# Performance work log

Hardware: AMD Instinct MI355X
Metric: run time of the kernel (lower is better)

Reference implementation:

```python
import jax, jax.numpy as jnp
import numpy as np

B, S, H, NH = 2, 1024, 1024, 16
SE, E = 512, 1024
NEXP, TOPK, FF = 8, 2, 2048
HD = H // NH
EPS = 1e-6
THETA = 10000.0
NEG = -1e9


def _rms(x, w):
    return x * jax.lax.rsqrt(jnp.mean(x * x, axis=-1, keepdims=True) + EPS) * w


def _rope(q, k, pos):
    # q,k: [B,S,NH,HD]; pos: [B,S] int
    inv = 1.0 / (THETA ** (jnp.arange(0, HD, 2, dtype=jnp.float32) / HD))
    f = pos[..., None].astype(jnp.float32) * inv            # [B,S,HD/2]
    emb = jnp.concatenate([f, f], axis=-1)                  # [B,S,HD]
    cos = jnp.cos(emb)[:, :, None, :]
    sin = jnp.sin(emb)[:, :, None, :]
    def rot(x):
        x1, x2 = jnp.split(x, 2, axis=-1)
        return jnp.concatenate([-x2, x1], axis=-1)
    return q * cos + rot(q) * sin, k * cos + rot(k) * sin


def _forward(hidden_states, encoder_hidden_states,
             in_ln_w, wq, wk, wv, wo,
             c_norm_w, cq_w, cq_b, ck_w, ck_b, cv_w, cv_b, co_w, co_b,
             post_ln_w, gate_w, w1, w2, w3,
             position_ids, encoder_attention_mask):
    x = hidden_states

    # ---- self-attention (RMSNorm pre-norm, RoPE, causal) ----
    res = x
    h = _rms(x, in_ln_w)
    q = (h @ wq.T).reshape(B, S, NH, HD)
    k = (h @ wk.T).reshape(B, S, NH, HD)
    v = (h @ wv.T).reshape(B, S, NH, HD)
    q, k = _rope(q, k, position_ids)
    scores = jnp.einsum('bqhd,bkhd->bhqk', q, k) / np.sqrt(HD)
    causal = jnp.tril(jnp.ones((S, S), dtype=bool))
    scores = jnp.where(causal, scores, NEG)
    attn = jax.nn.softmax(scores, axis=-1)
    o = jnp.einsum('bhqk,bkhd->bqhd', attn, v).reshape(B, S, H) @ wo.T
    x = res + o

    # ---- cross-attention block (RMSNorm, MHA with kdim=vdim=E, bias) ----
    res = x
    h = _rms(x, c_norm_w)
    cq = (h @ cq_w.T + cq_b).reshape(B, S, NH, HD)
    ck = (encoder_hidden_states @ ck_w.T + ck_b).reshape(B, SE, NH, HD)
    cv = (encoder_hidden_states @ cv_w.T + cv_b).reshape(B, SE, NH, HD)
    sc = jnp.einsum('bqhd,bkhd->bhqk', cq, ck) / np.sqrt(HD)
    pad = (encoder_attention_mask == 0)                     # key_padding_mask
    sc = jnp.where(pad[:, None, None, :], NEG, sc)
    ca = jax.nn.softmax(sc, axis=-1)
    o = jnp.einsum('bhqk,bkhd->bqhd', ca, cv).reshape(B, S, H) @ co_w.T + co_b
    x = res + o

    # ---- block-sparse MoE FFN (top-2 routing, SwiGLU experts) ----
    res = x
    h = _rms(x, post_ln_w).reshape(-1, H)                   # [T,H], T=B*S
    logits = h @ gate_w.T                                    # [T,NEXP]
    probs = jax.nn.softmax(logits, axis=-1)
    topv, topi = jax.lax.top_k(probs, TOPK)                  # [T,TOPK]
    topv = topv / jnp.sum(topv, axis=-1, keepdims=True)
    out = jnp.zeros_like(h)
    for e in range(NEXP):  # fixed small expert loop
        we = jnp.sum(jnp.where(topi == e, topv, 0.0), axis=-1)   # [T]
        ff = (jax.nn.silu(h @ w1[e].T) * (h @ w3[e].T)) @ w2[e].T
        out = out + we[:, None] * ff
    x = res + out.reshape(B, S, H)
    return x


def setup_inputs() -> dict:
    key = jax.random.key(0)
    ks = jax.random.split(key, 24)
    sc = 0.02
    d = {
        'hidden_states': jax.random.normal(ks[0], (B, S, H), jnp.float32),
        'position_ids': jnp.broadcast_to(jnp.arange(S, dtype=jnp.int64), (B, S)),
        'encoder_hidden_states': jax.random.normal(ks[1], (B, SE, E), jnp.float32),
        'encoder_attention_mask': jnp.ones((B, SE), jnp.int64),
        'in_ln_w': jnp.ones((H,), jnp.float32),
        'wq': jax.random.normal(ks[2], (H, H), jnp.float32) * sc,
        'wk': jax.random.normal(ks[3], (H, H), jnp.float32) * sc,
        'wv': jax.random.normal(ks[4], (H, H), jnp.float32) * sc,
        'wo': jax.random.normal(ks[5], (H, H), jnp.float32) * sc,
        'c_norm_w': jnp.ones((H,), jnp.float32),
        'cq_w': jax.random.normal(ks[6], (H, H), jnp.float32) * sc,
        'cq_b': jnp.zeros((H,), jnp.float32),
        'ck_w': jax.random.normal(ks[7], (H, E), jnp.float32) * sc,
        'ck_b': jnp.zeros((H,), jnp.float32),
        'cv_w': jax.random.normal(ks[8], (H, E), jnp.float32) * sc,
        'cv_b': jnp.zeros((H,), jnp.float32),
        'co_w': jax.random.normal(ks[9], (H, H), jnp.float32) * sc,
        'co_b': jnp.zeros((H,), jnp.float32),
        'post_ln_w': jnp.ones((H,), jnp.float32),
        'gate_w': jax.random.normal(ks[10], (NEXP, H), jnp.float32) * sc,
        'w1': jax.random.normal(ks[11], (NEXP, FF, H), jnp.float32) * sc,
        'w2': jax.random.normal(ks[12], (NEXP, H, FF), jnp.float32) * sc,
        'w3': jax.random.normal(ks[13], (NEXP, FF, H), jnp.float32) * sc,
    }
    return d


def reference(hidden_states, position_ids, encoder_hidden_states, encoder_attention_mask,
              in_ln_w, wq, wk, wv, wo,
              c_norm_w, cq_w, cq_b, ck_w, ck_b, cv_w, cv_b, co_w, co_b,
              post_ln_w, gate_w, w1, w2, w3):
    return _forward(hidden_states, encoder_hidden_states,
                    in_ln_w, wq, wk, wv, wo,
                    c_norm_w, cq_w, cq_b, ck_w, ck_b, cv_w, cv_b, co_w, co_b,
                    post_ln_w, gate_w, w1, w2, w3,
                    position_ids, encoder_attention_mask)
```

## Files before the change

kernel.cpp:

```cpp
#include <hip/hip_runtime.h>

#define B_    2
#define S_    1024
#define H_    1024
#define NH_   16
#define HD_   64
#define SE_   512
#define E_    1024
#define NEXP_ 8
#define FF_   2048
#define T_    (B_*S_)
#define TE_   (B_*SE_)
#define PERM_MAX 6400
#define MAXRT 24

typedef short v8s __attribute__((ext_vector_type(8)));
typedef short v4s __attribute__((ext_vector_type(4)));
typedef float v4f __attribute__((ext_vector_type(4)));
typedef _Float16 v8h __attribute__((ext_vector_type(8)));
typedef _Float16 v4h __attribute__((ext_vector_type(4)));

__device__ __forceinline__ unsigned short f2b(float f) {
  unsigned int u = __float_as_uint(f);
  u = (u + 0x7FFFu + ((u >> 16) & 1u)) >> 16;
  return (unsigned short)u;
}

__device__ __forceinline__ void g2l16(const void* g, void* l) {
  __builtin_amdgcn_global_load_lds(
      (const __attribute__((address_space(1))) unsigned int*)g,
      (__attribute__((address_space(3))) unsigned int*)l, 16, 0, 0);
}

__global__ void detect_kern(const int* __restrict__ pos, const int* __restrict__ msk,
                            int* __restrict__ flags) {
  if (threadIdx.x == 0) {
    flags[0] = (pos[1] == 1) ? 0 : 1;
    flags[1] = (msk[1] == 1) ? 0 : 1;
  }
}

struct SplitArgs {
  const float* src[9];
  _Float16* dh[9];
  _Float16* dl[9];
};
__global__ __launch_bounds__(256)
void split_all(SplitArgs sa) {
  int b = blockIdx.x;
  int seg, i;
  if (b < 4096) { seg = b >> 9; i = (b & 511) * 256 + threadIdx.x; }
  else          { seg = 8;      i = (b - 4096) * 256 + threadIdx.x; }
  const float* x = sa.src[seg];
  v4f a = *(const v4f*)&x[i * 8];
  v4f c = *(const v4f*)&x[i * 8 + 4];
  v8h hv, lv;
  #pragma unroll
  for (int j = 0; j < 8; ++j) {
    float v = j < 4 ? a[j] : c[j - 4];
    _Float16 hh = (_Float16)v;
    hv[j] = hh; lv[j] = (_Float16)(v - (float)hh);
  }
  *(v8h*)&sa.dh[seg][i * 8] = hv;
  *(v8h*)&sa.dl[seg][i * 8] = lv;
}

__global__ __launch_bounds__(256)
void cvt_all(const float* __restrict__ s0, const float* __restrict__ s1,
             const float* __restrict__ s2,
             unsigned short* __restrict__ d0, unsigned short* __restrict__ d1,
             unsigned short* __restrict__ d2) {
  int b = blockIdx.x;
  int seg = b >> 14;
  int i = (b & 16383) * 256 + threadIdx.x;
  const float* x = seg == 0 ? s0 : (seg == 1 ? s1 : s2);
  unsigned short* y = seg == 0 ? d0 : (seg == 1 ? d1 : d2);
  v4f v = *(const v4f*)&x[i * 4];
  v4s o;
  #pragma unroll
  for (int j = 0; j < 4; ++j) o[j] = (short)f2b(v[j]);
  *(v4s*)&y[i * 4] = o;
}

__global__ __launch_bounds__(256)
void rmsnorm_hl_kern(const float* __restrict__ x, const float* __restrict__ w,
                     _Float16* __restrict__ yh, _Float16* __restrict__ yl) {
  int row = blockIdx.x, tid = threadIdx.x;
  const float* xr = x + (long)row * 1024;
  v4f v = *(const v4f*)&xr[tid * 4];
  float ss = v[0]*v[0] + v[1]*v[1] + v[2]*v[2] + v[3]*v[3];
  #pragma unroll
  for (int off = 32; off; off >>= 1) ss += __shfl_xor(ss, off);
  __shared__ float sw[4];
  if ((tid & 63) == 0) sw[tid >> 6] = ss;
  __syncthreads();
  float tot = sw[0] + sw[1] + sw[2] + sw[3];
  float rs = rsqrtf(tot * (1.0f / 1024.0f) + 1e-6f);
  const float* wr = w + tid * 4;
  v4h oh, ol;
  #pragma unroll
  for (int j = 0; j < 4; ++j) {
    float f = v[j] * rs * wr[j];
    _Float16 hh = (_Float16)f;
    oh[j] = hh; ol[j] = (_Float16)(f - (float)hh);
  }
  *(v4h*)&yh[(long)row * 1024 + tid * 4] = oh;
  *(v4h*)&yl[(long)row * 1024 + tid * 4] = ol;
}

__global__ __launch_bounds__(256)
void rmsnorm_kern(const float* __restrict__ x, const float* __restrict__ w,
                  unsigned short* __restrict__ y) {
  int row = blockIdx.x, tid = threadIdx.x;
  const float* xr = x + (long)row * 1024;
  v4f v = *(const v4f*)&xr[tid * 4];
  float ss = v[0]*v[0] + v[1]*v[1] + v[2]*v[2] + v[3]*v[3];
  #pragma unroll
  for (int off = 32; off; off >>= 1) ss += __shfl_xor(ss, off);
  __shared__ float sw[4];
  if ((tid & 63) == 0) sw[tid >> 6] = ss;
  __syncthreads();
  float tot = sw[0] + sw[1] + sw[2] + sw[3];
  float rs = rsqrtf(tot * (1.0f / 1024.0f) + 1e-6f);
  const float* wr = w + tid * 4;
  v4s o;
  #pragma unroll
  for (int j = 0; j < 4; ++j) o[j] = (short)f2b(v[j] * rs * wr[j]);
  *(v4s*)&y[(long)row * 1024 + tid * 4] = o;
}

__global__ __launch_bounds__(256)
void rope_split_kern(float* __restrict__ q, const float* __restrict__ k,
                     _Float16* __restrict__ kh, _Float16* __restrict__ kl,
                     const int* __restrict__ pos, const int* __restrict__ flags) {
  int g = blockIdx.x * 256 + threadIdx.x;
  int d = g & 31;
  int h = (g >> 5) & 15;
  int s = (g >> 9) & (S_ - 1);
  int b = g >> 19;
  long base = (((long)(b * S_ + s)) * NH_ + h) * HD_;
  int pidx = b * S_ + s;
  int pv = pos[flags[0] ? (pidx << 1) : pidx];
  float p = (float)pv;
  float inv = powf(10000.0f, -(float)d * (1.0f / 32.0f));
  float f = p * inv;
  float sn = sinf(f), cs = cosf(f);
  float q1 = q[base + d], q2 = q[base + d + 32];
  q[base + d]      = q1 * cs - q2 * sn;
  q[base + d + 32] = q2 * cs + q1 * sn;
  float k1 = k[base + d], k2 = k[base + d + 32];
  float kr1 = k1 * cs - k2 * sn;
  float kr2 = k2 * cs + k1 * sn;
  _Float16 hh = (_Float16)kr1;
  kh[base + d] = hh; kl[base + d] = (_Float16)(kr1 - (float)hh);
  hh = (_Float16)kr2;
  kh[base + d + 32] = hh; kl[base + d + 32] = (_Float16)(kr2 - (float)hh);
}

__global__ __launch_bounds__(256)
void vtrans_kern(const float* __restrict__ vf, _Float16* __restrict__ vth,
                 _Float16* __restrict__ vtl, int Sk) {
  int kb = blockIdx.x, bh = blockIdx.y;
  int b = bh >> 4, h = bh & 15;
  int t = threadIdx.x;
  __shared__ float tile[64][65];
  int key = t >> 2, dsub = (t & 3) * 16;
  const float* src = vf + (((long)(b * Sk + kb * 64 + key)) * NH_ + h) * HD_ + dsub;
  #pragma unroll
  for (int j = 0; j < 16; j += 4) *(v4f*)&tile[key][dsub + j] = *(const v4f*)&src[j];
  __syncthreads();
  int d = t >> 2, ksub = (t & 3) * 16;
  v8h hv0, lv0, hv1, lv1;
  #pragma unroll
  for (int j = 0; j < 16; ++j) {
    float v = tile[ksub + j][d];
    _Float16 hh = (_Float16)v;
    if (j < 8) { hv0[j] = hh; lv0[j] = (_Float16)(v - (float)hh); }
    else       { hv1[j - 8] = hh; lv1[j - 8] = (_Float16)(v - (float)hh); }
  }
  long ob = (((long)(b * NH_ + h)) * HD_ + d) * Sk + kb * 64 + ksub;
  *(v8h*)&vth[ob] = hv0; *(v8h*)&vth[ob + 8] = hv1;
  *(v8h*)&vtl[ob] = lv0; *(v8h*)&vtl[ob + 8] = lv1;
}

struct ZArg {
  const _Float16 *Ah, *Al, *Bh, *Bl;
  const float *bias, *resid;
  float *Cf;
  _Float16 *Ch, *Cl;
  int M;
};

__global__ __launch_bounds__(256)
void gemm_hl(ZArg z0, ZArg z1, ZArg z2, int K) {
  ZArg za = blockIdx.z == 0 ? z0 : (blockIdx.z == 1 ? z1 : z2);
  int flat = blockIdx.x;
  int wg = (flat & 7) * 32 + (flat >> 3);
  int row0 = (wg >> 4) * 128;
  int col0 = (wg & 15) * 64;
  if (row0 >= za.M) return;
  int tid = threadIdx.x, lane = tid & 63, w = tid >> 6;
  int lr = lane & 15, lg = lane >> 4;
  int wr = w >> 1, wc = w & 1;
  int rsw = (lr >> 1) & 3;

  __shared__ _Float16 Ah_s[2][128 * 32], Al_s[2][128 * 32];
  __shared__ _Float16 Bh_s[2][64 * 32], Bl_s[2][64 * 32];

  int av0 = w * 64 + lane, av1 = (w + 4) * 64 + lane;
  int ar0 = av0 >> 2, as0 = (av0 & 3) ^ ((ar0 >> 1) & 3);
  int ar1 = av1 >> 2, as1 = (av1 & 3) ^ ((ar1 >> 1) & 3);
  int bv = w * 64 + lane;
  int br = bv >> 2, bs = (bv & 3) ^ ((br >> 1) & 3);
  const _Float16* ga0h = za.Ah + (long)(row0 + ar0) * K + as0 * 8;
  const _Float16* ga0l = za.Al + (long)(row0 + ar0) * K + as0 * 8;
  const _Float16* ga1h = za.Ah + (long)(row0 + ar1) * K + as1 * 8;
  const _Float16* ga1l = za.Al + (long)(row0 + ar1) * K + as1 * 8;
  const _Float16* gbh  = za.Bh + (long)(col0 + br) * K + bs * 8;
  const _Float16* gbl  = za.Bl + (long)(col0 + br) * K + bs * 8;

  auto stage = [&](int buf, int k0) {
    g2l16(ga0h + k0, (char*)Ah_s[buf] + w * 1024);
    g2l16(ga1h + k0, (char*)Ah_s[buf] + (w + 4) * 1024);
    g2l16(ga0l + k0, (char*)Al_s[buf] + w * 1024);
    g2l16(ga1l + k0, (char*)Al_s[buf] + (w + 4) * 1024);
    g2l16(gbh + k0, (char*)Bh_s[buf] + w * 1024);
    g2l16(gbl + k0, (char*)Bl_s[buf] + w * 1024);
  };

  v4f acc[4][2] = {};
  stage(0, 0);
  int cur = 0;

  for (int k0 = 0; k0 < K; k0 += 32) {
    __syncthreads();
    if (k0 + 32 < K) stage(cur ^ 1, k0 + 32);

    v8h ah[4], al[4], bh[2], bl[2];
    #pragma unroll
    for (int m = 0; m < 4; ++m) {
      int off = (wr * 64 + m * 16 + lr) * 64 + ((lg ^ rsw) << 4);
      ah[m] = *(const v8h*)((char*)Ah_s[cur] + off);
      al[m] = *(const v8h*)((char*)Al_s[cur] + off);
    }
    #pragma unroll
    for (int n = 0; n < 2; ++n) {
      int off = (wc * 32 + n * 16 + lr) * 64 + ((lg ^ rsw) << 4);
      bh[n] = *(const v8h*)((char*)Bh_s[cur] + off);
      bl[n] = *(const v8h*)((char*)Bl_s[cur] + off);
    }
    #pragma unroll
    for (int m = 0; m < 4; ++m)
      #pragma unroll
      for (int n = 0; n < 2; ++n) {
        acc[m][n] = __builtin_amdgcn_mfma_f32_16x16x32_f16(ah[m], bh[n], acc[m][n], 0, 0, 0);
        acc[m][n] = __builtin_amdgcn_mfma_f32_16x16x32_f16(ah[m], bl[n], acc[m][n], 0, 0, 0);
        acc[m][n] = __builtin_amdgcn_mfma_f32_16x16x32_f16(al[m], bh[n], acc[m][n], 0, 0, 0);
      }
    cur ^= 1;
  }

  #pragma unroll
  for (int m = 0; m < 4; ++m) {
    int rbase = row0 + wr * 64 + m * 16 + lg * 4;
    #pragma unroll
    for (int n = 0; n < 2; ++n) {
      int gcol = col0 + wc * 32 + n * 16 + lr;
      float bb = za.bias ? za.bias[gcol] : 0.0f;
      #pragma unroll
      for (int rr = 0; rr < 4; ++rr) {
        long idx = (long)(rbase + rr) * 1024 + gcol;
        float v = acc[m][n][rr] + bb;
        if (za.Cf) {
          za.Cf[idx] = za.resid ? (za.resid[idx] + v) : v;
        } else {
          _Float16 hh = (_Float16)v;
          za.Ch[idx] = hh;
          za.Cl[idx] = (_Float16)(v - (float)hh);
        }
      }
    }
  }
}

template<bool CAUSAL>
__global__ __launch_bounds__(256)
void attn_hl(const float* __restrict__ Q,
             const _Float16* __restrict__ Khg, const _Float16* __restrict__ Klg,
             const _Float16* __restrict__ Vhg, const _Float16* __restrict__ Vlg,
             _Float16* __restrict__ Oh, _Float16* __restrict__ Ol,
             const int* __restrict__ mask, const int* __restrict__ flags,
             int Sq, int Sk, float qscale) {
  int qt = blockIdx.x, bh = blockIdx.y;
  int b = bh >> 4, h = bh & 15;
  int tid = threadIdx.x, lane = tid & 63, w = tid >> 6;
  int lr = lane & 15, lg = lane >> 4;
  int q0 = qt * 64;
  int mf = (!CAUSAL && mask) ? flags[1] : 0;
  int swz = lr & 7;

  __shared__ _Float16 Kh_s[64 * 64], Kl_s[64 * 64];
  __shared__ _Float16 Vh_s[64 * 64], Vl_s[64 * 64];
  __shared__ _Float16 Psh[4][16][72], Psl[4][16][72];

  v8h qh[2], ql[2];
  {
    long qbase = ((long)(b * Sq + q0 + w * 16 + lr) * NH_ + h) * HD_;
    #pragma unroll
    for (int kk = 0; kk < 2; ++kk) {
      v4f f0 = *(const v4f*)&Q[qbase + kk * 32 + lg * 8];
      v4f f1 = *(const v4f*)&Q[qbase + kk * 32 + lg * 8 + 4];
      #pragma unroll
      for (int j = 0; j < 8; ++j) {
        float f = (j < 4 ? f0[j] : f1[j - 4]) * qscale;
        _Float16 hh = (_Float16)f;
        qh[kk][j] = hh;
        ql[kk][j] = (_Float16)(f - (float)hh);
      }
    }
  }
  v4f of[4] = {};
  float m4[4], l4[4];
  #pragma unroll
  for (int i = 0; i < 4; ++i) { m4[i] = -3e38f; l4[i] = 0.0f; }

  int nkt = CAUSAL ? (qt + 1) : (Sk >> 6);
  for (int kt = 0; kt < nkt; ++kt) {
    __syncthreads();
    #pragma unroll
    for (int i = 0; i < 2; ++i) {
      int c = w + i * 4;
      int v = c * 64 + lane;
      int row = v >> 3, c8 = v & 7;
      int sc = (c8 ^ (row & 7)) << 3;
      long kb = ((long)(b * Sk + kt * 64 + row) * NH_ + h) * HD_ + sc;
      g2l16(Khg + kb, (char*)Kh_s + c * 1024);
      g2l16(Klg + kb, (char*)Kl_s + c * 1024);
      long vb = ((long)(b * NH_ + h) * HD_ + row) * Sk + kt * 64 + sc;
      g2l16(Vhg + vb, (char*)Vh_s + c * 1024);
      g2l16(Vlg + vb, (char*)Vl_s + c * 1024);
    }
    __syncthreads();

    v4f sf[4] = {};
    #pragma unroll
    for (int kk = 0; kk < 2; ++kk)
      #pragma unroll
      for (int n = 0; n < 4; ++n) {
        int off = (n * 16 + lr) * 128 + ((((kk << 2) | lg) ^ swz) << 4);
        v8h kbh = *(const v8h*)((char*)Kh_s + off);
        v8h kbl = *(const v8h*)((char*)Kl_s + off);
        sf[n] = __builtin_amdgcn_mfma_f32_16x16x32_f16(qh[kk], kbh, sf[n], 0, 0, 0);
        sf[n] = __builtin_amdgcn_mfma_f32_16x16x32_f16(qh[kk], kbl, sf[n], 0, 0, 0);
        sf[n] = __builtin_amdgcn_mfma_f32_16x16x32_f16(ql[kk], kbh, sf[n], 0, 0, 0);
      }

    if constexpr (CAUSAL) {
      if (kt == qt) {
        #pragma unroll
        for (int n = 0; n < 4; ++n) {
          int kcol = kt * 64 + n * 16 + lr;
          #pragma unroll
          for (int rr = 0; rr < 4; ++rr) {
            int qr = q0 + w * 16 + lg * 4 + rr;
            if (kcol > qr) sf[n][rr] = -1e9f;
          }
        }
      }
    } else {
      if (mask) {
        #pragma unroll
        for (int n = 0; n < 4; ++n) {
          int kcol = kt * 64 + n * 16 + lr;
          int mi = b * Sk + kcol;
          if (mask[mf ? (mi << 1) : mi] == 0) {
            #pragma unroll
            for (int rr = 0; rr < 4; ++rr) sf[n][rr] = -1e9f;
          }
        }
      }
    }

    float al[4];
    #pragma unroll
    for (int rr = 0; rr < 4; ++rr) {
      float mx = fmaxf(fmaxf(sf[0][rr], sf[1][rr]), fmaxf(sf[2][rr], sf[3][rr]));
      #pragma unroll
      for (int off = 8; off; off >>= 1) mx = fmaxf(mx, __shfl_xor(mx, off));
      float mn = fmaxf(m4[rr], mx);
      al[rr] = __expf(m4[rr] - mn);
      m4[rr] = mn;
      float rs = 0.0f;
      #pragma unroll
      for (int n = 0; n < 4; ++n) {
        float pv = __expf(sf[n][rr] - mn);
        sf[n][rr] = pv;
        rs += pv;
      }
      #pragma unroll
      for (int off = 8; off; off >>= 1) rs += __shfl_xor(rs, off);
      l4[rr] = l4[rr] * al[rr] + rs;
    }

    #pragma unroll
    for (int n = 0; n < 4; ++n)
      #pragma unroll
      for (int rr = 0; rr < 4; ++rr) {
        of[n][rr] *= al[rr];
        float pv = sf[n][rr];
        _Float16 ph = (_Float16)pv;
        Psh[w][lg * 4 + rr][n * 16 + lr] = ph;
        Psl[w][lg * 4 + rr][n * 16 + lr] = (_Float16)(pv - (float)ph);
      }
    __syncthreads();

    #pragma unroll
    for (int kc = 0; kc < 2; ++kc) {
      v8h pah = *(const v8h*)&Psh[w][lr][kc * 32 + lg * 8];
      v8h pal = *(const v8h*)&Psl[w][lr][kc * 32 + lg * 8];
      #pragma unroll
      for (int n = 0; n < 4; ++n) {
        int off = (n * 16 + lr) * 128 + ((((kc << 2) | lg) ^ swz) << 4);
        v8h vbh = *(const v8h*)((char*)Vh_s + off);
        v8h vbl = *(const v8h*)((char*)Vl_s + off);
        of[n] = __builtin_amdgcn_mfma_f32_16x16x32_f16(pah, vbh, of[n], 0, 0, 0);
        of[n] = __builtin_amdgcn_mfma_f32_16x16x32_f16(pah, vbl, of[n], 0, 0, 0);
        of[n] = __builtin_amdgcn_mfma_f32_16x16x32_f16(pal, vbh, of[n], 0, 0, 0);
      }
    }
  }

  #pragma unroll
  for (int rr = 0; rr < 4; ++rr) {
    int qr = q0 + w * 16 + lg * 4 + rr;
    float inv = 1.0f / l4[rr];
    long ob = (long)(b * Sq + qr) * 1024 + h * 64;
    #pragma unroll
    for (int n = 0; n < 4; ++n) {
      float v = of[n][rr] * inv;
      _Float16 hh = (_Float16)v;
      Oh[ob + n * 16 + lr] = hh;
      Ol[ob + n * 16 + lr] = (_Float16)(v - (float)hh);
    }
  }
}

__global__ __launch_bounds__(512)
void moe_gemm1(const unsigned short* __restrict__ A,
               const unsigned short* __restrict__ B1,
               const unsigned short* __restrict__ B2,
               unsigned short* __restrict__ Cb,
               const int* __restrict__ tm_e, const int* __restrict__ tm_slot,
               const int* __restrict__ ntl, const int* __restrict__ perm) {
  int flat = blockIdx.x;
  int wg = (flat & 7) * 96 + (flat >> 3);
  int tile = wg >> 5;
  if (tile >= ntl[0]) return;
  int col0 = (wg & 31) * 64;
  int e = tm_e[tile];
  int row0 = tm_slot[tile];
  const unsigned short* Bp1 = B1 + (long)e * (FF_ * H_);
  const unsigned short* Bp2 = B2 + (long)e * (FF_ * H_);
  int tid = threadIdx.x, lane = tid & 63, w = tid >> 6;
  int lr = lane & 15, lg = lane >> 4;
  int wr = w >> 1, wc = w & 1;
  int rsw = (lr >> 1) & 3;

  __shared__ unsigned short As[2][256 * 32];
  __shared__ unsigned short Bs1[2][64 * 32];
  __shared__ unsigned short Bs2[2][64 * 32];

  const unsigned short* ga[2];
  #pragma unroll
  for (int i = 0; i < 2; ++i) {
    int c = i * 512 + tid;
    int r = c >> 2, sub = (c & 3) ^ ((r >> 1) & 3);
    int tok = perm[row0 + r];
    ga[i] = A + (long)(tok < 0 ? 0 : tok) * H_ + sub * 8;
  }
  int bc = tid & 255;
  int rb = bc >> 2, sb = (bc & 3) ^ ((rb >> 1) & 3);
  const unsigned short* gB = (tid < 256 ? Bp1 : Bp2) + (long)(col0 + rb) * H_ + sb * 8;
  size_t lBoff = (size_t)((w & 3) * 64) * 8;

  auto stage = [&](int buf, int k0) {
    #pragma unroll
    for (int i = 0; i < 2; ++i)
      g2l16(ga[i] + k0, As[buf] + (size_t)(i * 512 + w * 64) * 8);
    g2l16(gB + k0, (tid < 256 ? Bs1[buf] : Bs2[buf]) + lBoff);
  };

  v4f acc[4][2] = {};
  v4f acc2[4][2] = {};
  stage(0, 0);
  int cur = 0;

  for (int k0 = 0; k0 < H_; k0 += 32) {
    __syncthreads();
    if (k0 + 32 < H_) stage(cur ^ 1, k0 + 32);

    v8s a[4], b1[2], b2[2];
    #pragma unroll
    for (int m = 0; m < 4; ++m)
      a[m] = *(const v8s*)&As[cur][(wr * 64 + m * 16 + lr) * 32 + (lg ^ rsw) * 8];
    #pragma unroll
    for (int n = 0; n < 2; ++n) {
      b1[n] = *(const v8s*)&Bs1[cur][(wc * 32 + n * 16 + lr) * 32 + (lg ^ rsw) * 8];
      b2[n] = *(const v8s*)&Bs2[cur][(wc * 32 + n * 16 + lr) * 32 + (lg ^ rsw) * 8];
    }
    #pragma unroll
    for (int m = 0; m < 4; ++m)
      #pragma unroll
      for (int n = 0; n < 2; ++n) {
        acc[m][n]  = __builtin_amdgcn_mfma_f32_16x16x32_bf16(a[m], b1[n], acc[m][n], 0, 0, 0);
        acc2[m][n] = __builtin_amdgcn_mfma_f32_16x16x32_bf16(a[m], b2[n], acc2[m][n], 0, 0, 0);
      }
    cur ^= 1;
  }

  #pragma unroll
  for (int m = 0; m < 4; ++m) {
    int grow = row0 + wr * 64 + m * 16 + lg * 4;
    #pragma unroll
    for (int n = 0; n < 2; ++n) {
      int gcol = col0 + wc * 32 + n * 16 + lr;
      #pragma unroll
      for (int rr = 0; rr < 4; ++rr) {
        float v = acc[m][n][rr];
        float g = v / (1.0f + __expf(-v));
        Cb[(long)(grow + rr) * FF_ + gcol] = f2b(g * acc2[m][n][rr]);
      }
    }
  }
}

__global__ __launch_bounds__(256)
void moe_gemm2(const unsigned short* __restrict__ A,
               const unsigned short* __restrict__ B,
               float* __restrict__ Cf,
               const int* __restrict__ tm_e, const int* __restrict__ tm_slot,
               const int* __restrict__ ntl,
               const int* __restrict__ perm, const float* __restrict__ pwgt) {
  int flat = blockIdx.x;
  int wg = (flat & 7) * 96 + (flat >> 3);
  int t2 = wg >> 4;
  int tile = t2 >> 1;
  if (tile >= ntl[0]) return;
  int row0 = tm_slot[tile] + (t2 & 1) * 128;
  int col0 = (wg & 15) * 64;
  int e = tm_e[tile];
  const unsigned short* Bp = B + (long)e * (H_ * FF_);
  int tid = threadIdx.x, lane = tid & 63, w = tid >> 6;
  int lr = lane & 15, lg = lane >> 4;
  int rsw = (lr >> 1) & 3;

  __shared__ unsigned short As[2][128 * 32];
  __shared__ unsigned short Bs[2][64 * 32];

  const unsigned short* ga[2];
  #pragma unroll
  for (int i = 0; i < 2; ++i) {
    int c = i * 256 + tid;
    int r = c >> 2, sub = (c & 3) ^ ((r >> 1) & 3);
    ga[i] = A + (long)(row0 + r) * FF_ + sub * 8;
  }
  int rb = tid >> 2, sb = (tid & 3) ^ ((rb >> 1) & 3);
  const unsigned short* gb = Bp + (long)(col0 + rb) * FF_ + sb * 8;

  auto stage = [&](int buf, int k0) {
    #pragma unroll
    for (int i = 0; i < 2; ++i)
      g2l16(ga[i] + k0, As[buf] + (size_t)(i * 256 + w * 64) * 8);
    g2l16(gb + k0, Bs[buf] + (size_t)(w * 64) * 8);
  };

  v4f acc[2][4] = {};
  stage(0, 0);
  int cur = 0;

  for (int k0 = 0; k0 < FF_; k0 += 32) {
    __syncthreads();
    if (k0 + 32 < FF_) stage(cur ^ 1, k0 + 32);

    v8s a[2], b[4];
    #pragma unroll
    for (int m = 0; m < 2; ++m)
      a[m] = *(const v8s*)&As[cur][(w * 32 + m * 16 + lr) * 32 + (lg ^ rsw) * 8];
    #pragma unroll
    for (int n = 0; n < 4; ++n)
      b[n] = *(const v8s*)&Bs[cur][(n * 16 + lr) * 32 + (lg ^ rsw) * 8];
    #pragma unroll
    for (int m = 0; m < 2; ++m)
      #pragma unroll
      for (int n = 0; n < 4; ++n)
        acc[m][n] = __builtin_amdgcn_mfma_f32_16x16x32_bf16(a[m], b[n], acc[m][n], 0, 0, 0);
    cur ^= 1;
  }

  #pragma unroll
  for (int m = 0; m < 2; ++m) {
    int grow = row0 + w * 32 + m * 16 + lg * 4;
    #pragma unroll
    for (int rr = 0; rr < 4; ++rr) {
      int tok = perm[grow + rr];
      if (tok < 0) continue;
      float pw = pwgt[grow + rr];
      #pragma unroll
      for (int n = 0; n < 4; ++n) {
        int gcol = col0 + n * 16 + lr;
        atomicAdd(&Cf[(long)tok * H_ + gcol], acc[m][n][rr] * pw);
      }
    }
  }
}

__global__ __launch_bounds__(64)
void router_kern(const float* __restrict__ x, const float* __restrict__ w,
                 const float* __restrict__ gw,
                 int* __restrict__ topi, float* __restrict__ topw,
                 int* __restrict__ counts) {
  int t = blockIdx.x, lane = threadIdx.x;
  const float* xr = x + (long)t * 1024;
  float vals[16];
  float ss = 0.0f;
  #pragma unroll
  for (int i = 0; i < 16; ++i) { float v = xr[lane + i * 64]; vals[i] = v; ss += v * v; }
  #pragma unroll
  for (int off = 32; off; off >>= 1) ss += __shfl_xor(ss, off);
  float rs = rsqrtf(ss * (1.0f / 1024.0f) + 1e-6f);
  #pragma unroll
  for (int i = 0; i < 16; ++i) vals[i] *= rs * w[lane + i * 64];
  float lgts[8];
  #pragma unroll
  for (int e = 0; e < 8; ++e) {
    const float* g = gw + e * 1024;
    float s = 0.0f;
    #pragma unroll
    for (int i = 0; i < 16; ++i) s += vals[i] * g[lane + i * 64];
    #pragma unroll
    for (int off = 32; off; off >>= 1) s += __shfl_xor(s, off);
    lgts[e] = s;
  }
  int i1 = 0; float l1 = lgts[0];
  #pragma unroll
  for (int e = 1; e < 8; ++e) if (lgts[e] > l1) { l1 = lgts[e]; i1 = e; }
  int i2 = -1; float l2 = -3e38f;
  #pragma unroll
  for (int e = 0; e < 8; ++e) if (e != i1 && lgts[e] > l2) { l2 = lgts[e]; i2 = e; }
  float w1 = 1.0f / (1.0f + __expf(l2 - l1));
  if (lane == 0) {
    topi[t * 2] = i1; topi[t * 2 + 1] = i2;
    topw[t * 2] = w1; topw[t * 2 + 1] = 1.0f - w1;
    atomicAdd(&counts[i1], 1);
    atomicAdd(&counts[i2], 1);
  }
}

__global__ __launch_bounds__(256)
void finalize_kern(const int* __restrict__ counts, int* __restrict__ poff,
                   int* __restrict__ tm_e, int* __restrict__ tm_slot,
                   int* __restrict__ ntl, int* __restrict__ perm) {
  __shared__ int stot;
  if (threadIdx.x == 0) {
    int off = 0, nt = 0;
    for (int e = 0; e < 8; ++e) {
      poff[e] = off;
      int c = counts[e];
      int ntE = (c + 255) >> 8;
      for (int i = 0; i < ntE; ++i) { tm_e[nt] = e; tm_slot[nt] = off + i * 256; ++nt; }
      off += ntE * 256;
    }
    ntl[0] = nt; ntl[1] = off;
    stot = off;
  }
  __syncthreads();
  for (int s = threadIdx.x; s < stot; s += 256) perm[s] = -1;
}

__global__ __launch_bounds__(256)
void scatter_kern(const int* __restrict__ topi, const float* __restrict__ topw,
                  const int* __restrict__ poff, int* __restrict__ cursor,
                  int* __restrict__ perm, float* __restrict__ pwgt) {
  int t = blockIdx.x * 256 + threadIdx.x;
  if (t >= T_) return;
  #pragma unroll
  for (int kk = 0; kk < 2; ++kk) {
    int e = topi[t * 2 + kk];
    int pos = atomicAdd(&cursor[e], 1);
    int slot = poff[e] + pos;
    perm[slot] = t;
    pwgt[slot] = topw[t * 2 + kk];
  }
}

extern "C" void kernel_launch(void* const* d_in, const int* in_sizes, int n_in,
                              void* d_out, int out_size, void* d_ws, size_t ws_size,
                              hipStream_t stream) {
  (void)in_sizes; (void)n_in; (void)out_size; (void)ws_size;
  const float* x_in  = (const float*)d_in[0];
  const int*  posids = (const int*)d_in[1];
  const float* enc   = (const float*)d_in[2];
  const int*  emask  = (const int*)d_in[3];
  const float* inln  = (const float*)d_in[4];
  const float* wq    = (const float*)d_in[5];
  const float* wk    = (const float*)d_in[6];
  const float* wv    = (const float*)d_in[7];
  const float* wo    = (const float*)d_in[8];
  const float* cnorm = (const float*)d_in[9];
  const float* cqw   = (const float*)d_in[10];
  const float* cqb   = (const float*)d_in[11];
  const float* ckw   = (const float*)d_in[12];
  const float* ckb   = (const float*)d_in[13];
  const float* cvw   = (const float*)d_in[14];
  const float* cvb   = (const float*)d_in[15];
  const float* cow   = (const float*)d_in[16];
  const float* cob   = (const float*)d_in[17];
  const float* pln   = (const float*)d_in[18];
  const float* gatew = (const float*)d_in[19];
  const float* w1    = (const float*)d_in[20];
  const float* w2    = (const float*)d_in[21];
  const float* w3    = (const float*)d_in[22];
  float* out = (float*)d_out;

  char* p = (char*)d_ws;
  auto alloc = [&](size_t bytes) -> char* {
    char* r = p;
    p += (bytes + 255) & ~(size_t)255;
    return r;
  };
  const size_t MB = 1024 * 1024;
  char* A1 = alloc(4 * MB);
  char* A2 = alloc(4 * MB);
  char* Bq = alloc(8 * MB);
  char* Bk = alloc(8 * MB);
  char* Bv = alloc(8 * MB);
  char* C1 = alloc(4 * MB);
  char* C2 = alloc(4 * MB);
  char* D1 = alloc(4 * MB);
  char* D2 = alloc(4 * MB);
  float* x1 = (float*)alloc(8 * MB);
  float* x2 = (float*)alloc(8 * MB);
  unsigned short* h3b = (unsigned short*)alloc(4 * MB);
  _Float16* ench = (_Float16*)alloc(2 * MB);
  _Float16* encl = (_Float16*)alloc(2 * MB);
  int*   meta    = (int*)alloc(4 * (8 + 8 + 8 + 2 + 2 + MAXRT + MAXRT));
  int*   counts  = meta;
  int*   cursor  = meta + 8;
  int*   poff    = meta + 16;
  int*   ntl     = meta + 24;
  int*   flags   = meta + 26;
  int*   tm_e    = meta + 28;
  int*   tm_slot = meta + 28 + MAXRT;
  int*   topi    = (int*)alloc((size_t)T_ * 2 * 4);
  float* topw    = (float*)alloc((size_t)T_ * 2 * 4);
  int*   perm    = (int*)alloc((size_t)PERM_MAX * 4);
  float* pwgt    = (float*)alloc((size_t)PERM_MAX * 4);
  unsigned short* w1b = (unsigned short*)alloc((size_t)NEXP_ * FF_ * H_ * 2);
  unsigned short* w3b = (unsigned short*)alloc((size_t)NEXP_ * FF_ * H_ * 2);
  unsigned short* w2b = (unsigned short*)alloc((size_t)NEXP_ * H_ * FF_ * 2);

  _Float16 *hh = (_Float16*)A1, *hl = (_Float16*)A2;
  _Float16 *oh = (_Float16*)A1, *ol = (_Float16*)A2;
  _Float16 *ckh = (_Float16*)A1, *ckl = (_Float16*)A2;
  float* qf = (float*)Bq;  float* cqf = (float*)Bq;
  float* kf = (float*)Bk;
  _Float16 *cvth = (_Float16*)Bk, *cvtl = (_Float16*)(Bk + 4 * MB);
  float* vf = (float*)Bv;  float* cvf = (float*)Bv;
  _Float16 *kh = (_Float16*)C1, *kl = (_Float16*)C2;
  _Float16 *h2h = (_Float16*)C1, *h2l = (_Float16*)C2;
  _Float16 *vth = (_Float16*)D1, *vtl = (_Float16*)D2;
  _Float16 *coh = (_Float16*)D1, *col = (_Float16*)D2;
  unsigned short* ffh = (unsigned short*)Bq;
  _Float16* wsp = (_Float16*)w1b;
  auto wsph = [&](int i) { return wsp + (size_t)i * 2097152; };
  auto wspl = [&](int i) { return wsp + (size_t)i * 2097152 + 1048576; };

  dim3 blk(256);

  detect_kern<<<1, 64, 0, stream>>>(posids, emask, flags);

  {
    SplitArgs sa;
    const float* wlist[8] = {wq, wk, wv, wo, cqw, ckw, cvw, cow};
    for (int i = 0; i < 8; ++i) { sa.src[i] = wlist[i]; sa.dh[i] = wsph(i); sa.dl[i] = wspl(i); }
    sa.src[8] = enc; sa.dh[8] = ench; sa.dl[8] = encl;
    split_all<<<4608, blk, 0, stream>>>(sa);
  }

  rmsnorm_hl_kern<<<T_, blk, 0, stream>>>(x_in, inln, hh, hl);
  {
    ZArg zq = {hh, hl, wsph(0), wspl(0), nullptr, nullptr, qf, nullptr, nullptr, 2048};
    ZArg zk = {hh, hl, wsph(1), wspl(1), nullptr, nullptr, kf, nullptr, nullptr, 2048};
    ZArg zv = {hh, hl, wsph(2), wspl(2), nullptr, nullptr, vf, nullptr, nullptr, 2048};
    gemm_hl<<<dim3(256, 1, 3), blk, 0, stream>>>(zq, zk, zv, 1024);
  }
  rope_split_kern<<<(B_ * S_ * NH_ * 32) / 256, blk, 0, stream>>>(qf, kf, kh, kl, posids, flags);
  vtrans_kern<<<dim3(16, 32), blk, 0, stream>>>(vf, vth, vtl, 1024);
  attn_hl<true><<<dim3(16, 32), blk, 0, stream>>>(
      qf, kh, kl, vth, vtl, oh, ol, nullptr, flags, 1024, 1024, 0.125f);
  {
    ZArg zo = {oh, ol, wsph(3), wspl(3), nullptr, x_in, x1, nullptr, nullptr, 2048};
    gemm_hl<<<dim3(256, 1, 1), blk, 0, stream>>>(zo, zo, zo, 1024);
  }

  rmsnorm_hl_kern<<<T_, blk, 0, stream>>>(x1, cnorm, h2h, h2l);
  {
    ZArg zcq = {h2h, h2l, wsph(4), wspl(4), cqb, nullptr, cqf, nullptr, nullptr, 2048};
    ZArg zck = {ench, encl, wsph(5), wspl(5), ckb, nullptr, nullptr, ckh, ckl, 1024};
    ZArg zcv = {ench, encl, wsph(6), wspl(6), cvb, nullptr, cvf, nullptr, nullptr, 1024};
    gemm_hl<<<dim3(256, 1, 3), blk, 0, stream>>>(zcq, zck, zcv, 1024);
  }
  vtrans_kern<<<dim3(8, 32), blk, 0, stream>>>(cvf, cvth, cvtl, 512);
  attn_hl<false><<<dim3(16, 32), blk, 0, stream>>>(
      cqf, ckh, ckl, cvth, cvtl, coh, col, emask, flags, 1024, 512, 0.125f);
  {
    ZArg zco = {coh, col, wsph(7), wspl(7), cob, x1, x2, nullptr, nullptr, 2048};
    gemm_hl<<<dim3(256, 1, 1), blk, 0, stream>>>(zco, zco, zco, 1024);
  }

  cvt_all<<<49152, blk, 0, stream>>>(w1, w3, w2, w1b, w3b, w2b);
  rmsnorm_kern<<<T_, blk, 0, stream>>>(x2, pln, h3b);
  hipMemsetAsync(meta, 0, 64, stream);
  router_kern<<<T_, dim3(64), 0, stream>>>(x2, pln, gatew, topi, topw, counts);
  finalize_kern<<<1, blk, 0, stream>>>(counts, poff, tm_e, tm_slot, ntl, perm);
  scatter_kern<<<(T_ + 255) / 256, blk, 0, stream>>>(topi, topw, poff, cursor, perm, pwgt);
  moe_gemm1<<<768, dim3(512), 0, stream>>>(
      h3b, w1b, w3b, ffh, tm_e, tm_slot, ntl, perm);
  hipMemcpyAsync(out, x2, (size_t)T_ * H_ * 4, hipMemcpyDeviceToDevice, stream);
  moe_gemm2<<<768, blk, 0, stream>>>(
      ffh, w2b, out, tm_e, tm_slot, ntl, perm, pwgt);
}
```

Baseline: 568.6 us.

## Triple-buffer LDS staging with explicit vmcnt waits in three GEMM kernels

Switches the split-fp16 dense GEMM and both MoE expert GEMMs from double- to triple-buffered LDS staging, prefetching two k-steps ahead. The __syncthreads per iteration is replaced by a partial s_waitcnt vmcnt plus a raw s_barrier, so loads for later stages stay in flight while the current stage is consumed. This aims to hide global-to-LDS latency at the cost of more shared memory per block, which may lower occupancy. It also relies on the vmcnt counts exactly matching the number of async loads issued per stage.

```diff
diff --git a/kernel.cpp b/kernel.cpp
--- a/kernel.cpp
+++ b/kernel.cpp
@@ -204,8 +204,8 @@
   int wr = w >> 1, wc = w & 1;
   int rsw = (lr >> 1) & 3;
 
-  __shared__ _Float16 Ah_s[2][128 * 32], Al_s[2][128 * 32];
-  __shared__ _Float16 Bh_s[2][64 * 32], Bl_s[2][64 * 32];
+  __shared__ _Float16 Ah_s[3][128 * 32], Al_s[3][128 * 32];
+  __shared__ _Float16 Bh_s[3][64 * 32], Bl_s[3][64 * 32];
 
   int av0 = w * 64 + lane, av1 = (w + 4) * 64 + lane;
   int ar0 = av0 >> 2, as0 = (av0 & 3) ^ ((ar0 >> 1) & 3);
@@ -229,12 +229,17 @@
   };
 
   v4f acc[4][2] = {};
+  int nk = K >> 5;
   stage(0, 0);
-  int cur = 0;
-
-  for (int k0 = 0; k0 < K; k0 += 32) {
-    __syncthreads();
-    if (k0 + 32 < K) stage(cur ^ 1, k0 + 32);
+  stage(1, 32);
+
+  for (int it = 0; it < nk; ++it) {
+    if (it == nk - 1) asm volatile("s_waitcnt vmcnt(0)" ::: "memory");
+    else              asm volatile("s_waitcnt vmcnt(6)" ::: "memory");
+    __builtin_amdgcn_s_barrier();
+    asm volatile("" ::: "memory");
+    if (it + 2 < nk) stage((it + 2) % 3, (it + 2) << 5);
+    int cur = it % 3;
 
     v8h ah[4], al[4], bh[2], bl[2];
     #pragma unroll
@@ -257,7 +262,6 @@
         acc[m][n] = __builtin_amdgcn_mfma_f32_16x16x32_f16(ah[m], bl[n], acc[m][n], 0, 0, 0);
         acc[m][n] = __builtin_amdgcn_mfma_f32_16x16x32_f16(al[m], bh[n], acc[m][n], 0, 0, 0);
       }
-    cur ^= 1;
   }
 
   #pragma unroll
@@ -466,9 +470,9 @@
   int wr = w >> 1, wc = w & 1;
   int rsw = (lr >> 1) & 3;
 
-  __shared__ unsigned short As[2][256 * 32];
-  __shared__ unsigned short Bs1[2][64 * 32];
-  __shared__ unsigned short Bs2[2][64 * 32];
+  __shared__ unsigned short As[3][256 * 32];
+  __shared__ unsigned short Bs1[3][64 * 32];
+  __shared__ unsigned short Bs2[3][64 * 32];
 
   const unsigned short* ga[2];
   #pragma unroll
@@ -492,12 +496,17 @@
 
   v4f acc[4][2] = {};
   v4f acc2[4][2] = {};
+  const int nk = 32;
   stage(0, 0);
-  int cur = 0;
-
-  for (int k0 = 0; k0 < H_; k0 += 32) {
-    __syncthreads();
-    if (k0 + 32 < H_) stage(cur ^ 1, k0 + 32);
+  stage(1, 32);
+
+  for (int it = 0; it < nk; ++it) {
+    if (it == nk - 1) asm volatile("s_waitcnt vmcnt(0)" ::: "memory");
+    else              asm volatile("s_waitcnt vmcnt(3)" ::: "memory");
+    __builtin_amdgcn_s_barrier();
+    asm volatile("" ::: "memory");
+    if (it + 2 < nk) stage((it + 2) % 3, (it + 2) << 5);
+    int cur = it % 3;
 
     v8s a[4], b1[2], b2[2];
     #pragma unroll
@@ -515,7 +524,6 @@
         acc[m][n]  = __builtin_amdgcn_mfma_f32_16x16x32_bf16(a[m], b1[n], acc[m][n], 0, 0, 0);
         acc2[m][n] = __builtin_amdgcn_mfma_f32_16x16x32_bf16(a[m], b2[n], acc2[m][n], 0, 0, 0);
       }
-    cur ^= 1;
   }
 
   #pragma unroll
@@ -554,8 +562,8 @@
   int lr = lane & 15, lg = lane >> 4;
   int rsw = (lr >> 1) & 3;
 
-  __shared__ unsigned short As[2][128 * 32];
-  __shared__ unsigned short Bs[2][64 * 32];
+  __shared__ unsigned short As[3][128 * 32];
+  __shared__ unsigned short Bs[3][64 * 32];
 
   const unsigned short* ga[2];
   #pragma unroll
@@ -575,12 +583,17 @@
   };
 
   v4f acc[2][4] = {};
+  const int nk = 64;
   stage(0, 0);
-  int cur = 0;
-
-  for (int k0 = 0; k0 < FF_; k0 += 32) {
-    __syncthreads();
-    if (k0 + 32 < FF_) stage(cur ^ 1, k0 + 32);
+  stage(1, 32);
+
+  for (int it = 0; it < nk; ++it) {
+    if (it == nk - 1) asm volatile("s_waitcnt vmcnt(0)" ::: "memory");
+    else              asm volatile("s_waitcnt vmcnt(3)" ::: "memory");
+    __builtin_amdgcn_s_barrier();
+    asm volatile("" ::: "memory");
+    if (it + 2 < nk) stage((it + 2) % 3, (it + 2) << 5);
+    int cur = it % 3;
 
     v8s a[2], b[4];
     #pragma unroll
@@ -594,7 +607,6 @@
       #pragma unroll
       for (int n = 0; n < 4; ++n)
         acc[m][n] = __builtin_amdgcn_mfma_f32_16x16x32_bf16(a[m], b[n], acc[m][n], 0, 0, 0);
-    cur ^= 1;
   }
 
   #pragma unroll
```

New measurement: 615.9 us. 8.3% more time.

## Fuse routing finalize and scatter, dual-write residual, drop memset and memcpy

Applied to the files above, without the earlier changes.

Zeroing of the routing counters moves into the detect kernel, so the separate memset is gone. The finalize and scatter kernels become one single-block kernel that uses shared-memory cursors. The cross-attention output GEMM now writes its result to both x2 and the final output buffer, which removes the 8 MB device-to-device copy. The attention launch also becomes a flat 1D grid with a swizzled block mapping to improve L2 locality. The trade-off is that the scatter now runs serially in a single block over 4096 entries, and every output element of that GEMM is stored twice.

```diff
diff --git a/kernel.cpp b/kernel.cpp
--- a/kernel.cpp
+++ b/kernel.cpp
@@ -33,7 +33,8 @@
 }
 
 __global__ void detect_kern(const int* __restrict__ pos, const int* __restrict__ msk,
-                            int* __restrict__ flags) {
+                            int* __restrict__ flags, int* __restrict__ counts) {
+  if (threadIdx.x < 16) counts[threadIdx.x] = 0;
   if (threadIdx.x == 0) {
     flags[0] = (pos[1] == 1) ? 0 : 1;
     flags[1] = (msk[1] == 1) ? 0 : 1;
@@ -187,6 +188,7 @@
   const _Float16 *Ah, *Al, *Bh, *Bl;
   const float *bias, *resid;
   float *Cf;
+  float *Cf2;
   _Float16 *Ch, *Cl;
   int M;
 };
@@ -272,7 +274,9 @@
         long idx = (long)(rbase + rr) * 1024 + gcol;
         float v = acc[m][n][rr] + bb;
         if (za.Cf) {
-          za.Cf[idx] = za.resid ? (za.resid[idx] + v) : v;
+          float r = za.resid ? (za.resid[idx] + v) : v;
+          za.Cf[idx] = r;
+          if (za.Cf2) za.Cf2[idx] = r;
         } else {
           _Float16 hh = (_Float16)v;
           za.Ch[idx] = hh;
@@ -291,7 +295,9 @@
              _Float16* __restrict__ Oh, _Float16* __restrict__ Ol,
              const int* __restrict__ mask, const int* __restrict__ flags,
              int Sq, int Sk, float qscale) {
-  int qt = blockIdx.x, bh = blockIdx.y;
+  int flat = blockIdx.x;
+  int wgA = (flat & 7) * 64 + (flat >> 3);
+  int qt = wgA & 15, bh = wgA >> 4;
   int b = bh >> 4, h = bh & 15;
   int tid = threadIdx.x, lane = tid & 63, w = tid >> 6;
   int lr = lane & 15, lg = lane >> 4;
@@ -657,14 +663,20 @@
 }
 
 __global__ __launch_bounds__(256)
-void finalize_kern(const int* __restrict__ counts, int* __restrict__ poff,
-                   int* __restrict__ tm_e, int* __restrict__ tm_slot,
-                   int* __restrict__ ntl, int* __restrict__ perm) {
+void route_pack_kern(const int* __restrict__ counts,
+                     const int* __restrict__ topi, const float* __restrict__ topw,
+                     int* __restrict__ poff,
+                     int* __restrict__ tm_e, int* __restrict__ tm_slot,
+                     int* __restrict__ ntl,
+                     int* __restrict__ perm, float* __restrict__ pwgt) {
+  __shared__ int s_poff[8];
+  __shared__ int s_cur[8];
   __shared__ int stot;
+  if (threadIdx.x < 8) s_cur[threadIdx.x] = 0;
   if (threadIdx.x == 0) {
     int off = 0, nt = 0;
     for (int e = 0; e < 8; ++e) {
-      poff[e] = off;
+      s_poff[e] = off; poff[e] = off;
       int c = counts[e];
       int ntE = (c + 255) >> 8;
       for (int i = 0; i < ntE; ++i) { tm_e[nt] = e; tm_slot[nt] = off + i * 256; ++nt; }
@@ -675,21 +687,16 @@
   }
   __syncthreads();
   for (int s = threadIdx.x; s < stot; s += 256) perm[s] = -1;
-}
-
-__global__ __launch_bounds__(256)
-void scatter_kern(const int* __restrict__ topi, const float* __restrict__ topw,
-                  const int* __restrict__ poff, int* __restrict__ cursor,
-                  int* __restrict__ perm, float* __restrict__ pwgt) {
-  int t = blockIdx.x * 256 + threadIdx.x;
-  if (t >= T_) return;
-  #pragma unroll
-  for (int kk = 0; kk < 2; ++kk) {
-    int e = topi[t * 2 + kk];
-    int pos = atomicAdd(&cursor[e], 1);
-    int slot = poff[e] + pos;
-    perm[slot] = t;
-    pwgt[slot] = topw[t * 2 + kk];
+  __syncthreads();
+  for (int t = threadIdx.x; t < T_; t += 256) {
+    #pragma unroll
+    for (int kk = 0; kk < 2; ++kk) {
+      int e = topi[t * 2 + kk];
+      int pos = atomicAdd(&s_cur[e], 1);
+      int slot = s_poff[e] + pos;
+      perm[slot] = t;
+      pwgt[slot] = topw[t * 2 + kk];
+    }
   }
 }
 
@@ -745,7 +752,6 @@
   _Float16* encl = (_Float16*)alloc(2 * MB);
   int*   meta    = (int*)alloc(4 * (8 + 8 + 8 + 2 + 2 + MAXRT + MAXRT));
   int*   counts  = meta;
-  int*   cursor  = meta + 8;
   int*   poff    = meta + 16;
   int*   ntl     = meta + 24;
   int*   flags   = meta + 26;
@@ -777,7 +783,7 @@
 
   dim3 blk(256);
 
-  detect_kern<<<1, 64, 0, stream>>>(posids, emask, flags);
+  detect_kern<<<1, 64, 0, stream>>>(posids, emask, flags, counts);
 
   {
     SplitArgs sa;
@@ -789,44 +795,42 @@
 
   rmsnorm_hl_kern<<<T_, blk, 0, stream>>>(x_in, inln, hh, hl);
   {
-    ZArg zq = {hh, hl, wsph(0), wspl(0), nullptr, nullptr, qf, nullptr, nullptr, 2048};
-    ZArg zk = {hh, hl, wsph(1), wspl(1), nullptr, nullptr, kf, nullptr, nullptr, 2048};
-    ZArg zv = {hh, hl, wsph(2), wspl(2), nullptr, nullptr, vf, nullptr, nullptr, 2048};
+    ZArg zq = {hh, hl, wsph(0), wspl(0), nullptr, nullptr, qf, nullptr, nullptr, nullptr, 2048};
+    ZArg zk = {hh, hl, wsph(1), wspl(1), nullptr, nullptr, kf, nullptr, nullptr, nullptr, 2048};
+    ZArg zv = {hh, hl, wsph(2), wspl(2), nullptr, nullptr, vf, nullptr, nullptr, nullptr, 2048};
     gemm_hl<<<dim3(256, 1, 3), blk, 0, stream>>>(zq, zk, zv, 1024);
   }
   rope_split_kern<<<(B_ * S_ * NH_ * 32) / 256, blk, 0, stream>>>(qf, kf, kh, kl, posids, flags);
   vtrans_kern<<<dim3(16, 32), blk, 0, stream>>>(vf, vth, vtl, 1024);
-  attn_hl<true><<<dim3(16, 32), blk, 0, stream>>>(
+  attn_hl<true><<<512, blk, 0, stream>>>(
       qf, kh, kl, vth, vtl, oh, ol, nullptr, flags, 1024, 1024, 0.125f);
   {
-    ZArg zo = {oh, ol, wsph(3), wspl(3), nullptr, x_in, x1, nullptr, nullptr, 2048};
+    ZArg zo = {oh, ol, wsph(3), wspl(3), nullptr, x_in, x1, nullptr, nullptr, nullptr, 2048};
     gemm_hl<<<dim3(256, 1, 1), blk, 0, stream>>>(zo, zo, zo, 1024);
   }
 
   rmsnorm_hl_kern<<<T_, blk, 0, stream>>>(x1, cnorm, h2h, h2l);
   {
-    ZArg zcq = {h2h, h2l, wsph(4), wspl(4), cqb, nullptr, cqf, nullptr, nullptr, 2048};
-    ZArg zck = {ench, encl, wsph(5), wspl(5), ckb, nullptr, nullptr, ckh, ckl, 1024};
-    ZArg zcv = {ench, encl, wsph(6), wspl(6), cvb, nullptr, cvf, nullptr, nullptr, 1024};
+    ZArg zcq = {h2h, h2l, wsph(4), wspl(4), cqb, nullptr, cqf, nullptr, nullptr, nullptr, 2048};
+    ZArg zck = {ench, encl, wsph(5), wspl(5), ckb, nullptr, nullptr, nullptr, ckh, ckl, 1024};
+    ZArg zcv = {ench, encl, wsph(6), wspl(6), cvb, nullptr, cvf, nullptr, nullptr, nullptr, 1024};
     gemm_hl<<<dim3(256, 1, 3), blk, 0, stream>>>(zcq, zck, zcv, 1024);
   }
   vtrans_kern<<<dim3(8, 32), blk, 0, stream>>>(cvf, cvth, cvtl, 512);
-  attn_hl<false><<<dim3(16, 32), blk, 0, stream>>>(
+  attn_hl<false><<<512, blk, 0, stream>>>(
       cqf, ckh, ckl, cvth, cvtl, coh, col, emask, flags, 1024, 512, 0.125f);
   {
-    ZArg zco = {coh, col, wsph(7), wspl(7), cob, x1, x2, nullptr, nullptr, 2048};
+    ZArg zco = {coh, col, wsph(7), wspl(7), cob, x1, x2, out, nullptr, nullptr, 2048};
     gemm_hl<<<dim3(256, 1, 1), blk, 0, stream>>>(zco, zco, zco, 1024);
   }
 
   cvt_all<<<49152, blk, 0, stream>>>(w1, w3, w2, w1b, w3b, w2b);
   rmsnorm_kern<<<T_, blk, 0, stream>>>(x2, pln, h3b);
-  hipMemsetAsync(meta, 0, 64, stream);
   router_kern<<<T_, dim3(64), 0, stream>>>(x2, pln, gatew, topi, topw, counts);
-  finalize_kern<<<1, blk, 0, stream>>>(counts, poff, tm_e, tm_slot, ntl, perm);
-  scatter_kern<<<(T_ + 255) / 256, blk, 0, stream>>>(topi, topw, poff, cursor, perm, pwgt);
+  route_pack_kern<<<1, blk, 0, stream>>>(counts, topi, topw, poff, tm_e, tm_slot,
+                                         ntl, perm, pwgt);
   moe_gemm1<<<768, dim3(512), 0, stream>>>(
       h3b, w1b, w3b, ffh, tm_e, tm_slot, ntl, perm);
-  hipMemcpyAsync(out, x2, (size_t)T_ * H_ * 4, hipMemcpyDeviceToDevice, stream);
   moe_gemm2<<<768, blk, 0, stream>>>(
       ffh, w2b, out, tm_e, tm_slot, ntl, perm, pwgt);
 }
```

Result: faster. 539.1 us, median of 2 (-5.2%).
